# Kernel optimization log

Hardware: AMD Instinct MI355X
Metric: run time of the kernel (lower is better)

Reference implementation:

```python
import jax, jax.numpy as jnp
from jax import lax
import numpy as np

SCALE = 1.0   # self.scale
EPS = 1e-12
CHUNK = 512   # points processed per chunk to bound [P,T,3] temporaries


def _closest_sqdist(p, a, b, c):
    """Squared distance from points p:[P,3] to triangles (a,b,c):[T,3] -> [P,T].
    Ericson's closest-point-on-triangle, fully vectorized."""
    ab = b - a
    ac = c - a
    bc = c - b
    ap = p[:, None, :] - a[None, :, :]
    bp = p[:, None, :] - b[None, :, :]
    cp = p[:, None, :] - c[None, :, :]
    d1 = jnp.einsum('td,ptd->pt', ab, ap)
    d2 = jnp.einsum('td,ptd->pt', ac, ap)
    d3 = jnp.einsum('td,ptd->pt', ab, bp)
    d4 = jnp.einsum('td,ptd->pt', ac, bp)
    d5 = jnp.einsum('td,ptd->pt', ab, cp)
    d6 = jnp.einsum('td,ptd->pt', ac, cp)
    va = d3 * d6 - d5 * d4
    vb = d5 * d2 - d1 * d6
    vc = d1 * d4 - d3 * d2

    def sdiv(n, d):  # NaN/Inf-safe division (branch is masked out by where anyway)
        return n / jnp.where(jnp.abs(d) < EPS, 1.0, d)

    t_ab = sdiv(d1, d1 - d3)[..., None]
    t_ac = sdiv(d2, d2 - d6)[..., None]
    t_bc = sdiv(d4 - d3, (d4 - d3) + (d5 - d6))[..., None]
    denom = va + vb + vc
    v_in = sdiv(vb, denom)[..., None]
    w_in = sdiv(vc, denom)[..., None]

    # base case: interior of the face; then overwrite with edge / vertex regions
    cl = a[None] + v_in * ab[None] + w_in * ac[None]
    cl = jnp.where(((va <= 0) & (d4 - d3 >= 0) & (d5 - d6 >= 0))[..., None],
                   b[None] + t_bc * bc[None], cl)   # edge BC
    cl = jnp.where(((vb <= 0) & (d2 >= 0) & (d6 <= 0))[..., None],
                   a[None] + t_ac * ac[None], cl)   # edge AC
    cl = jnp.where(((vc <= 0) & (d1 >= 0) & (d3 <= 0))[..., None],
                   a[None] + t_ab * ab[None], cl)   # edge AB
    cl = jnp.where(((d6 >= 0) & (d5 <= d6))[..., None], c[None], cl)  # vertex C
    cl = jnp.where(((d3 >= 0) & (d4 <= d3))[..., None], b[None], cl)  # vertex B
    cl = jnp.where(((d1 <= 0) & (d2 <= 0))[..., None], a[None], cl)   # vertex A
    diff = p[:, None, :] - cl
    return jnp.sum(diff * diff, axis=-1)


def setup_inputs():
    key = jax.random.key(0)
    k1, k2, k3 = jax.random.split(key, 3)
    vertices = jax.random.normal(k1, (4, 3, 16, 16, 16), dtype=jnp.float32)
    pc = jax.random.uniform(k2, (4, 4096, 3), dtype=jnp.float32)
    faces = jax.random.randint(k3, (8192, 3), 0, 4096, dtype=jnp.int32)
    return {"vertices": vertices, "pc": pc, "faces": faces}


def reference(vertices, pc, faces):
    B = vertices.shape[0]
    v = jax.nn.sigmoid(vertices)                     # self.normalization
    pos = jnp.moveaxis(v, 1, -1).reshape(B, -1, 3)   # permute(1,2,3,0).view(-1,3)
    pts = pc * SCALE                                 # _scale_points
    # pymesh path drops all-zero points; emulate with a mask (scaling keeps zeros zero)
    mask = jnp.any(pc != 0.0, axis=-1).astype(pts.dtype)  # [B,N]

    def per_batch(args):
        posb, pb, mb = args
        a = posb[faces[:, 0]]
        b = posb[faces[:, 1]]
        c = posb[faces[:, 2]]
        n_chunks = pb.shape[0] // CHUNK

        def chunk_min(pch):  # [CHUNK,3] -> [CHUNK] nearest sq-dist over all tris
            return jnp.min(_closest_sqdist(pch, a, b, c), axis=-1)

        d = lax.map(chunk_min, pb.reshape(n_chunks, CHUNK, 3)).reshape(-1)
        cnt = jnp.maximum(jnp.sum(mb), 1.0)
        return jnp.sum(d * mb) / cnt                 # mean(squared_distances)

    losses = lax.map(per_batch, (pos, pts, mask))    # [B]
    return jnp.mean(losses)
```

## Files before the change

kernel.cpp:

```cpp
#include <hip/hip_runtime.h>
#include <math.h>
#include <float.h>

#define NB 4
#define NP 4096
#define NT 8192
#define NS 64
#define TCH (NT/NS)
#define TREC 20
#define EPSD 1e-12

typedef float f2 __attribute__((ext_vector_type(2)));

__device__ __forceinline__ float sigm(float x) { return 1.0f / (1.0f + expf(-x)); }
__device__ __forceinline__ f2 vmin2(f2 a, f2 b) { return __builtin_elementwise_min(a, b); }
__device__ __forceinline__ f2 vmax2(f2 a, f2 b) { return __builtin_elementwise_max(a, b); }
__device__ __forceinline__ f2 clamp01(f2 x) {
  f2 z; z.x = 0.0f; z.y = 0.0f;
  f2 o; o.x = 1.0f; o.y = 1.0f;
  return vmin2(vmax2(x, z), o);
}

__global__ __launch_bounds__(256) void prep_kernel(
    const float* __restrict__ verts, const int* __restrict__ faces,
    float* __restrict__ tri)
{
  int idx = blockIdx.x * 256 + threadIdx.x;
  if (idx >= NB * NT) return;
  int b = idx >> 13;
  int t = idx & (NT - 1);
  int f0 = faces[3 * t + 0], f1 = faces[3 * t + 1], f2i = faces[3 * t + 2];
  const float* vb = verts + (size_t)b * 3 * NP;
  float ax = sigm(vb[f0]),  ay = sigm(vb[NP + f0]),  az = sigm(vb[2 * NP + f0]);
  float bx = sigm(vb[f1]),  by = sigm(vb[NP + f1]),  bz = sigm(vb[2 * NP + f1]);
  float cx = sigm(vb[f2i]), cy = sigm(vb[NP + f2i]), cz = sigm(vb[2 * NP + f2i]);
  float abx = bx - ax, aby = by - ay, abz = bz - az;
  float acx = cx - ax, acy = cy - ay, acz = cz - az;
  double aa = (double)abx * abx + (double)aby * aby + (double)abz * abz;
  double am = (double)abx * acx + (double)aby * acy + (double)abz * acz;
  double cc = (double)acx * acx + (double)acy * acy + (double)acz * acz;
  double den = aa * cc - am * am;
  double bb  = aa - 2.0 * am + cc;
  float raa  = (fabs(aa)  < EPSD) ? 1.0f : (float)(1.0 / aa);
  float rcc  = (fabs(cc)  < EPSD) ? 1.0f : (float)(1.0 / cc);
  float rbb  = (fabs(bb)  < EPSD) ? 1.0f : (float)(1.0 / bb);
  float rden = (fabs(den) < EPSD) ? 0.0f : (float)(1.0 / den);
  float* r = tri + (size_t)idx * TREC;
  r[0]  = ax;  r[1]  = ay;  r[2]  = az;
  r[3]  = abx; r[4]  = aby; r[5]  = abz;
  r[6]  = acx; r[7]  = acy; r[8]  = acz;
  r[9]  = (float)aa; r[10] = (float)am; r[11] = (float)cc;
  r[12] = raa; r[13] = rcc; r[14] = rbb; r[15] = rden;
  r[16] = (float)den; r[17] = (float)bb; r[18] = (float)(aa - am); r[19] = 0.0f;
}

__global__ __launch_bounds__(256) void dist_kernel(
    const float* __restrict__ tri, const float* __restrict__ pc,
    float* __restrict__ part)
{
  int bid  = blockIdx.x;
  int pblk = bid & 7;
  int s    = (bid >> 3) & (NS - 1);
  int b    = bid >> 9;
  int p0   = pblk * 512 + threadIdx.x;
  const float* pp0 = pc + ((size_t)b * NP + p0) * 3;
  const float* pp1 = pp0 + 256 * 3;
  f2 px, py, pz;
  px.x = pp0[0]; px.y = pp1[0];
  py.x = pp0[1]; py.y = pp1[1];
  pz.x = pp0[2]; pz.y = pp1[2];

  const float4* __restrict__ R =
      (const float4*)(tri + (size_t)(b * NT + s * TCH) * TREC);
  f2 mind; mind.x = FLT_MAX; mind.y = FLT_MAX;

  #pragma unroll 2
  for (int t = 0; t < TCH; ++t) {
    float4 r0 = R[0], r1 = R[1], r2 = R[2], r3 = R[3], r4 = R[4];
    R += 5;
    float abx = r0.w, aby = r1.x, abz = r1.y;
    float acx = r1.z, acy = r1.w, acz = r2.x;
    float aa = r2.y, am = r2.z, cc = r2.w;
    float raa = r3.x, rcc = r3.y, rbb = r3.z, rden = r3.w;
    float den = r4.x, bb = r4.y, k1 = r4.z;

    f2 apx = px - r0.x, apy = py - r0.y, apz = pz - r0.z;

    f2 d1   = apx * abx + apy * aby + apz * abz;
    f2 d2   = apx * acx + apy * acy + apz * acz;
    f2 apap = apx * apx + apy * apy + apz * apz;

    f2 vb = d1 * cc - d2 * am;
    f2 vc = d2 * aa - d1 * am;
    f2 va = den - vb - vc;

    f2 di = apap - (vb * d1 + vc * d2) * rden;

    f2 t2 = d1 + d1;
    f2 tab = clamp01(d1 * raa);
    f2 dAB = apap + tab * (tab * aa - t2);

    f2 t4 = d2 + d2;
    f2 tac = clamp01(d2 * rcc);
    f2 dAC = apap + tac * (tac * cc - t4);

    f2 e = d2 - d1 + k1;
    f2 tbc = clamp01(e * rbb);
    f2 distB = apap - t2 + aa;
    f2 dBC = distB + tbc * (tbc * bb - (e + e));

    f2 m3 = vmin2(vmin2(dAB, dAC), dBC);

    bool in0 = (vb.x >= 0.0f) & (vc.x >= 0.0f) & (va.x > 0.0f);
    bool in1 = (vb.y >= 0.0f) & (vc.y >= 0.0f) & (va.y > 0.0f);
    f2 dist;
    dist.x = in0 ? di.x : m3.x;
    dist.y = in1 ? di.y : m3.y;

    mind = vmin2(mind, dist);
  }
  float* dst = part + ((size_t)b * NS + s) * NP + p0;
  dst[0]   = fmaxf(mind.x, 0.0f);
  dst[256] = fmaxf(mind.y, 0.0f);
}

__global__ __launch_bounds__(256) void reduce_kernel(
    const float* __restrict__ part, const float* __restrict__ pc,
    float* __restrict__ bl2)
{
  int blk = blockIdx.x;
  int b = blk >> 4;
  int p = (blk & 15) * 256 + threadIdx.x;
  float m = FLT_MAX;
  #pragma unroll
  for (int s = 0; s < NS; ++s)
    m = fminf(m, part[((size_t)b * NS + s) * NP + p]);
  const float* pp = pc + ((size_t)b * NP + p) * 3;
  float x = pp[0], y = pp[1], z = pp[2];
  float msk = ((x != 0.0f) | (y != 0.0f) | (z != 0.0f)) ? 1.0f : 0.0f;
  float sdm = m * msk, sm = msk;
  for (int off = 32; off > 0; off >>= 1) {
    sdm += __shfl_down(sdm, off, 64);
    sm  += __shfl_down(sm,  off, 64);
  }
  __shared__ float s1[4], s2[4];
  int wave = threadIdx.x >> 6, lane = threadIdx.x & 63;
  if (lane == 0) { s1[wave] = sdm; s2[wave] = sm; }
  __syncthreads();
  if (threadIdx.x == 0) {
    bl2[2 * blk]     = s1[0] + s1[1] + s1[2] + s1[3];
    bl2[2 * blk + 1] = s2[0] + s2[1] + s2[2] + s2[3];
  }
}

__global__ void final_kernel(const float* __restrict__ bl2, float* __restrict__ out)
{
  if (threadIdx.x == 0 && blockIdx.x == 0) {
    float acc = 0.0f;
    for (int b = 0; b < NB; ++b) {
      float sdm = 0.0f, sm = 0.0f;
      for (int k = 0; k < 16; ++k) {
        sdm += bl2[2 * (b * 16 + k)];
        sm  += bl2[2 * (b * 16 + k) + 1];
      }
      acc += sdm / fmaxf(sm, 1.0f);
    }
    out[0] = 0.25f * acc;
  }
}

extern "C" void kernel_launch(void* const* d_in, const int* in_sizes, int n_in,
                              void* d_out, int out_size, void* d_ws, size_t ws_size,
                              hipStream_t stream) {
  const float* verts = (const float*)d_in[0];
  const float* pc    = (const float*)d_in[1];
  const int*   faces = (const int*)d_in[2];
  float* out = (float*)d_out;

  float* tri  = (float*)d_ws;
  float* part = tri  + (size_t)NB * NT * TREC;
  float* bl2  = part + (size_t)NB * NS * NP;

  prep_kernel<<<(NB * NT) / 256, 256, 0, stream>>>(verts, faces, tri);
  dist_kernel<<<NB * NS * 8, 256, 0, stream>>>(tri, pc, part);
  reduce_kernel<<<NB * 16, 256, 0, stream>>>(part, pc, bl2);
  final_kernel<<<1, 64, 0, stream>>>(bl2, out);
}
```

Measured before the change: 180.2 us.

## Fuse triangle prep, distance, and reduction into one kernel using atomics

Replaces the four-kernel pipeline with a single kernel. Each block computes its own triangle records into shared memory, reduces its per-point minima into global memory with atomicMin on the float bits, and lets the last-arriving block, found through an atomic counter, compute the final loss. Each thread now handles four points and each block covers 64 triangles instead of 128. This removes the global triangle buffer, the large partial-minimum array and several launches. In exchange it adds a memset, atomic traffic, and redundant per-block triangle preparation with double-precision math.

```diff
diff --git a/kernel.cpp b/kernel.cpp
--- a/kernel.cpp
+++ b/kernel.cpp
@@ -5,167 +5,163 @@
 #define NB 4
 #define NP 4096
 #define NT 8192
-#define NS 64
+#define NS 128
 #define TCH (NT/NS)
-#define TREC 20
+#define GRID (NB*NS*4)
 #define EPSD 1e-12
+#define CINIT 0x7F7F7F7Fu
 
 typedef float f2 __attribute__((ext_vector_type(2)));
 
 __device__ __forceinline__ float sigm(float x) { return 1.0f / (1.0f + expf(-x)); }
-__device__ __forceinline__ f2 vmin2(f2 a, f2 b) { return __builtin_elementwise_min(a, b); }
-__device__ __forceinline__ f2 vmax2(f2 a, f2 b) { return __builtin_elementwise_max(a, b); }
-__device__ __forceinline__ f2 clamp01(f2 x) {
-  f2 z; z.x = 0.0f; z.y = 0.0f;
-  f2 o; o.x = 1.0f; o.y = 1.0f;
-  return vmin2(vmax2(x, z), o);
+
+__device__ __forceinline__ void tri_point(
+    float4 r0, float4 r1, float4 r2, float4 r3, float4 r4,
+    f2 px, f2 py, f2 pz, f2& mind)
+{
+  float abx = r0.w, aby = r1.x, abz = r1.y;
+  float acx = r1.z, acy = r1.w, acz = r2.x;
+  float aa = r2.y, am = r2.z, cc = r2.w;
+  float raa = r3.x, rcc = r3.y, rbb = r3.z, rden = r3.w;
+  float den = r4.x, bb = r4.y, k1 = r4.z;
+
+  f2 apx = px - r0.x, apy = py - r0.y, apz = pz - r0.z;
+  f2 d1   = apx * abx + apy * aby + apz * abz;
+  f2 d2   = apx * acx + apy * acy + apz * acz;
+  f2 apap = apx * apx + apy * apy + apz * apz;
+
+  f2 vb = d1 * cc - d2 * am;
+  f2 vc = d2 * aa - d1 * am;
+  f2 va = den - vb - vc;
+  f2 di = apap - (vb * d1 + vc * d2) * rden;
+
+  f2 t2  = d1 + d1;
+  f2 uab = d1 * raa;
+  f2 tab; tab.x = fminf(fmaxf(uab.x, 0.0f), 1.0f);
+          tab.y = fminf(fmaxf(uab.y, 0.0f), 1.0f);
+  f2 dAB = apap + tab * (tab * aa - t2);
+
+  f2 t4  = d2 + d2;
+  f2 uac = d2 * rcc;
+  f2 tac; tac.x = fminf(fmaxf(uac.x, 0.0f), 1.0f);
+          tac.y = fminf(fmaxf(uac.y, 0.0f), 1.0f);
+  f2 dAC = apap + tac * (tac * cc - t4);
+
+  f2 e   = d2 - d1 + k1;
+  f2 ubc = e * rbb;
+  f2 tbc; tbc.x = fminf(fmaxf(ubc.x, 0.0f), 1.0f);
+          tbc.y = fminf(fmaxf(ubc.y, 0.0f), 1.0f);
+  f2 distB = apap - t2 + aa;
+  f2 e2 = e + e;
+  f2 dBC = distB + tbc * (tbc * bb - e2);
+
+  float m3x = fminf(fminf(dAB.x, dAC.x), dBC.x);
+  float m3y = fminf(fminf(dAB.y, dAC.y), dBC.y);
+  float sx  = fminf(fminf(vb.x, vc.x), va.x);
+  float sy  = fminf(fminf(vb.y, vc.y), va.y);
+  float dx = (sx > 0.0f) ? di.x : m3x;
+  float dy = (sy > 0.0f) ? di.y : m3y;
+  mind.x = fminf(mind.x, dx);
+  mind.y = fminf(mind.y, dy);
 }
 
-__global__ __launch_bounds__(256) void prep_kernel(
-    const float* __restrict__ verts, const int* __restrict__ faces,
-    float* __restrict__ tri)
+__global__ __launch_bounds__(256) void mega_kernel(
+    const float* __restrict__ verts, const float* __restrict__ pc,
+    const int* __restrict__ faces, unsigned int* __restrict__ part2,
+    unsigned int* __restrict__ counter, float* __restrict__ out)
 {
-  int idx = blockIdx.x * 256 + threadIdx.x;
-  if (idx >= NB * NT) return;
-  int b = idx >> 13;
-  int t = idx & (NT - 1);
-  int f0 = faces[3 * t + 0], f1 = faces[3 * t + 1], f2i = faces[3 * t + 2];
-  const float* vb = verts + (size_t)b * 3 * NP;
-  float ax = sigm(vb[f0]),  ay = sigm(vb[NP + f0]),  az = sigm(vb[2 * NP + f0]);
-  float bx = sigm(vb[f1]),  by = sigm(vb[NP + f1]),  bz = sigm(vb[2 * NP + f1]);
-  float cx = sigm(vb[f2i]), cy = sigm(vb[NP + f2i]), cz = sigm(vb[2 * NP + f2i]);
-  float abx = bx - ax, aby = by - ay, abz = bz - az;
-  float acx = cx - ax, acy = cy - ay, acz = cz - az;
-  double aa = (double)abx * abx + (double)aby * aby + (double)abz * abz;
-  double am = (double)abx * acx + (double)aby * acy + (double)abz * acz;
-  double cc = (double)acx * acx + (double)acy * acy + (double)acz * acz;
-  double den = aa * cc - am * am;
-  double bb  = aa - 2.0 * am + cc;
-  float raa  = (fabs(aa)  < EPSD) ? 1.0f : (float)(1.0 / aa);
-  float rcc  = (fabs(cc)  < EPSD) ? 1.0f : (float)(1.0 / cc);
-  float rbb  = (fabs(bb)  < EPSD) ? 1.0f : (float)(1.0 / bb);
-  float rden = (fabs(den) < EPSD) ? 0.0f : (float)(1.0 / den);
-  float* r = tri + (size_t)idx * TREC;
-  r[0]  = ax;  r[1]  = ay;  r[2]  = az;
-  r[3]  = abx; r[4]  = aby; r[5]  = abz;
-  r[6]  = acx; r[7]  = acy; r[8]  = acz;
-  r[9]  = (float)aa; r[10] = (float)am; r[11] = (float)cc;
-  r[12] = raa; r[13] = rcc; r[14] = rbb; r[15] = rden;
-  r[16] = (float)den; r[17] = (float)bb; r[18] = (float)(aa - am); r[19] = 0.0f;
-}
+  __shared__ float4 rec[TCH][5];
+  __shared__ unsigned int is_last;
+  __shared__ float red[8];
 
-__global__ __launch_bounds__(256) void dist_kernel(
-    const float* __restrict__ tri, const float* __restrict__ pc,
-    float* __restrict__ part)
-{
   int bid  = blockIdx.x;
-  int pblk = bid & 7;
-  int s    = (bid >> 3) & (NS - 1);
+  int pblk = bid & 3;
+  int s    = (bid >> 2) & (NS - 1);
   int b    = bid >> 9;
-  int p0   = pblk * 512 + threadIdx.x;
-  const float* pp0 = pc + ((size_t)b * NP + p0) * 3;
-  const float* pp1 = pp0 + 256 * 3;
-  f2 px, py, pz;
-  px.x = pp0[0]; px.y = pp1[0];
-  py.x = pp0[1]; py.y = pp1[1];
-  pz.x = pp0[2]; pz.y = pp1[2];
+  int tid  = threadIdx.x;
 
-  const float4* __restrict__ R =
-      (const float4*)(tri + (size_t)(b * NT + s * TCH) * TREC);
-  f2 mind; mind.x = FLT_MAX; mind.y = FLT_MAX;
+  if (tid < TCH) {
+    int t = s * TCH + tid;
+    int f0 = faces[3 * t + 0], f1 = faces[3 * t + 1], f2i = faces[3 * t + 2];
+    const float* vv = verts + (size_t)b * 3 * NP;
+    float ax = sigm(vv[f0]),  ay = sigm(vv[NP + f0]),  az = sigm(vv[2 * NP + f0]);
+    float bx = sigm(vv[f1]),  by = sigm(vv[NP + f1]),  bz = sigm(vv[2 * NP + f1]);
+    float cx = sigm(vv[f2i]), cy = sigm(vv[NP + f2i]), cz = sigm(vv[2 * NP + f2i]);
+    float abx = bx - ax, aby = by - ay, abz = bz - az;
+    float acx = cx - ax, acy = cy - ay, acz = cz - az;
+    double aa = (double)abx * abx + (double)aby * aby + (double)abz * abz;
+    double am = (double)abx * acx + (double)aby * acy + (double)abz * acz;
+    double cc = (double)acx * acx + (double)acy * acy + (double)acz * acz;
+    double den = aa * cc - am * am;
+    double bb  = aa - 2.0 * am + cc;
+    float raa  = (fabs(aa)  < EPSD) ? 1.0f : (float)(1.0 / aa);
+    float rcc  = (fabs(cc)  < EPSD) ? 1.0f : (float)(1.0 / cc);
+    float rbb  = (fabs(bb)  < EPSD) ? 1.0f : (float)(1.0 / bb);
+    float rden = (fabs(den) < EPSD) ? 0.0f : (float)(1.0 / den);
+    rec[tid][0] = make_float4(ax, ay, az, abx);
+    rec[tid][1] = make_float4(aby, abz, acx, acy);
+    rec[tid][2] = make_float4(acz, (float)aa, (float)am, (float)cc);
+    rec[tid][3] = make_float4(raa, rcc, rbb, rden);
+    rec[tid][4] = make_float4((float)den, (float)bb, (float)(aa - am), 0.0f);
+  }
+  __syncthreads();
+
+  int p0 = pblk * 1024 + tid;
+  const float* pp = pc + ((size_t)b * NP + p0) * 3;
+  f2 pxA, pyA, pzA, pxB, pyB, pzB;
+  pxA.x = pp[0];    pyA.x = pp[1];    pzA.x = pp[2];
+  pxA.y = pp[768];  pyA.y = pp[769];  pzA.y = pp[770];
+  pxB.x = pp[1536]; pyB.x = pp[1537]; pzB.x = pp[1538];
+  pxB.y = pp[2304]; pyB.y = pp[2305]; pzB.y = pp[2306];
+  f2 mindA, mindB;
+  mindA.x = mindA.y = mindB.x = mindB.y = 3.0e38f;
 
   #pragma unroll 2
   for (int t = 0; t < TCH; ++t) {
-    float4 r0 = R[0], r1 = R[1], r2 = R[2], r3 = R[3], r4 = R[4];
-    R += 5;
-    float abx = r0.w, aby = r1.x, abz = r1.y;
-    float acx = r1.z, acy = r1.w, acz = r2.x;
-    float aa = r2.y, am = r2.z, cc = r2.w;
-    float raa = r3.x, rcc = r3.y, rbb = r3.z, rden = r3.w;
-    float den = r4.x, bb = r4.y, k1 = r4.z;
+    float4 r0 = rec[t][0], r1 = rec[t][1], r2 = rec[t][2],
+           r3 = rec[t][3], r4 = rec[t][4];
+    tri_point(r0, r1, r2, r3, r4, pxA, pyA, pzA, mindA);
+    tri_point(r0, r1, r2, r3, r4, pxB, pyB, pzB, mindB);
+  }
 
-    f2 apx = px - r0.x, apy = py - r0.y, apz = pz - r0.z;
+  unsigned int* dst = part2 + b * NP + p0;
+  atomicMin(dst,       __float_as_uint(fmaxf(mindA.x, 0.0f)));
+  atomicMin(dst + 256, __float_as_uint(fmaxf(mindA.y, 0.0f)));
+  atomicMin(dst + 512, __float_as_uint(fmaxf(mindB.x, 0.0f)));
+  atomicMin(dst + 768, __float_as_uint(fmaxf(mindB.y, 0.0f)));
 
-    f2 d1   = apx * abx + apy * aby + apz * abz;
-    f2 d2   = apx * acx + apy * acy + apz * acz;
-    f2 apap = apx * apx + apy * apy + apz * apz;
-
-    f2 vb = d1 * cc - d2 * am;
-    f2 vc = d2 * aa - d1 * am;
-    f2 va = den - vb - vc;
-
-    f2 di = apap - (vb * d1 + vc * d2) * rden;
-
-    f2 t2 = d1 + d1;
-    f2 tab = clamp01(d1 * raa);
-    f2 dAB = apap + tab * (tab * aa - t2);
-
-    f2 t4 = d2 + d2;
-    f2 tac = clamp01(d2 * rcc);
-    f2 dAC = apap + tac * (tac * cc - t4);
-
-    f2 e = d2 - d1 + k1;
-    f2 tbc = clamp01(e * rbb);
-    f2 distB = apap - t2 + aa;
-    f2 dBC = distB + tbc * (tbc * bb - (e + e));
-
-    f2 m3 = vmin2(vmin2(dAB, dAC), dBC);
-
-    bool in0 = (vb.x >= 0.0f) & (vc.x >= 0.0f) & (va.x > 0.0f);
-    bool in1 = (vb.y >= 0.0f) & (vc.y >= 0.0f) & (va.y > 0.0f);
-    f2 dist;
-    dist.x = in0 ? di.x : m3.x;
-    dist.y = in1 ? di.y : m3.y;
-
-    mind = vmin2(mind, dist);
+  __threadfence();
+  if (tid == 0) {
+    unsigned int old = atomicAdd(counter, 1u);
+    is_last = (old == CINIT + (unsigned)GRID - 1u) ? 1u : 0u;
   }
-  float* dst = part + ((size_t)b * NS + s) * NP + p0;
-  dst[0]   = fmaxf(mind.x, 0.0f);
-  dst[256] = fmaxf(mind.y, 0.0f);
-}
-
-__global__ __launch_bounds__(256) void reduce_kernel(
-    const float* __restrict__ part, const float* __restrict__ pc,
-    float* __restrict__ bl2)
-{
-  int blk = blockIdx.x;
-  int b = blk >> 4;
-  int p = (blk & 15) * 256 + threadIdx.x;
-  float m = FLT_MAX;
-  #pragma unroll
-  for (int s = 0; s < NS; ++s)
-    m = fminf(m, part[((size_t)b * NS + s) * NP + p]);
-  const float* pp = pc + ((size_t)b * NP + p) * 3;
-  float x = pp[0], y = pp[1], z = pp[2];
-  float msk = ((x != 0.0f) | (y != 0.0f) | (z != 0.0f)) ? 1.0f : 0.0f;
-  float sdm = m * msk, sm = msk;
-  for (int off = 32; off > 0; off >>= 1) {
-    sdm += __shfl_down(sdm, off, 64);
-    sm  += __shfl_down(sm,  off, 64);
-  }
-  __shared__ float s1[4], s2[4];
-  int wave = threadIdx.x >> 6, lane = threadIdx.x & 63;
-  if (lane == 0) { s1[wave] = sdm; s2[wave] = sm; }
   __syncthreads();
-  if (threadIdx.x == 0) {
-    bl2[2 * blk]     = s1[0] + s1[1] + s1[2] + s1[3];
-    bl2[2 * blk + 1] = s2[0] + s2[1] + s2[2] + s2[3];
-  }
-}
-
-__global__ void final_kernel(const float* __restrict__ bl2, float* __restrict__ out)
-{
-  if (threadIdx.x == 0 && blockIdx.x == 0) {
-    float acc = 0.0f;
-    for (int b = 0; b < NB; ++b) {
+  if (is_last) {
+    __threadfence();
+    float loss = 0.0f;
+    for (int bb = 0; bb < NB; ++bb) {
       float sdm = 0.0f, sm = 0.0f;
-      for (int k = 0; k < 16; ++k) {
-        sdm += bl2[2 * (b * 16 + k)];
-        sm  += bl2[2 * (b * 16 + k) + 1];
+      for (int p = tid; p < NP; p += 256) {
+        unsigned int u = __hip_atomic_load(&part2[bb * NP + p],
+                                           __ATOMIC_RELAXED, __HIP_MEMORY_SCOPE_AGENT);
+        float m = __uint_as_float(u);
+        const float* q = pc + ((size_t)bb * NP + p) * 3;
+        bool nz = (q[0] != 0.0f) | (q[1] != 0.0f) | (q[2] != 0.0f);
+        if (nz) { sdm += m; sm += 1.0f; }
       }
-      acc += sdm / fmaxf(sm, 1.0f);
+      for (int off = 32; off > 0; off >>= 1) {
+        sdm += __shfl_down(sdm, off, 64);
+        sm  += __shfl_down(sm,  off, 64);
+      }
+      int wv = tid >> 6, ln = tid & 63;
+      if (ln == 0) { red[wv] = sdm; red[4 + wv] = sm; }
+      __syncthreads();
+      if (tid == 0)
+        loss += (red[0] + red[1] + red[2] + red[3]) /
+                fmaxf(red[4] + red[5] + red[6] + red[7], 1.0f);
+      __syncthreads();
     }
-    out[0] = 0.25f * acc;
+    if (tid == 0) out[0] = 0.25f * loss;
   }
 }
 
@@ -177,12 +173,9 @@
   const int*   faces = (const int*)d_in[2];
   float* out = (float*)d_out;
 
-  float* tri  = (float*)d_ws;
-  float* part = tri  + (size_t)NB * NT * TREC;
-  float* bl2  = part + (size_t)NB * NS * NP;
+  unsigned int* part2   = (unsigned int*)d_ws;
+  unsigned int* counter = part2 + NB * NP;
 
-  prep_kernel<<<(NB * NT) / 256, 256, 0, stream>>>(verts, faces, tri);
-  dist_kernel<<<NB * NS * 8, 256, 0, stream>>>(tri, pc, part);
-  reduce_kernel<<<NB * 16, 256, 0, stream>>>(part, pc, bl2);
-  final_kernel<<<1, 64, 0, stream>>>(bl2, out);
+  hipMemsetAsync(d_ws, 0x7F, (size_t)NB * NP * 4 + 4, stream);
+  mega_kernel<<<GRID, 256, 0, stream>>>(verts, pc, faces, part2, counter, out);
 }
```

New measurement: 223.8 us. 24.2% more time.
